# Optimization experiments

Measured on AMD Instinct MI355X. Metric: run time of the kernel, lower is better.

## Reference

```python
import jax, jax.numpy as jnp
import numpy as np

EMB_DIM = 1024
NUM_HEAD = 16
HEAD_DIM = EMB_DIM // NUM_HEAD
B, S = 2, 2048


def setup_inputs() -> dict:
    key = jax.random.key(0)
    ks = jax.random.split(key, 10)
    scale = 1.0 / np.sqrt(EMB_DIM)
    x = jax.random.normal(ks[0], (B, S, EMB_DIM), dtype=jnp.float32)
    # causal mask: 1 = keep, 0 = masked out (torch masked_fill(mask == 0, -inf))
    mask = jnp.tril(jnp.ones((S, S), dtype=jnp.int32))[None, None, :, :]
    def lin(kw, kb):
        W = jax.random.uniform(kw, (EMB_DIM, EMB_DIM), jnp.float32, -scale, scale)
        b = jax.random.uniform(kb, (EMB_DIM,), jnp.float32, -scale, scale)
        return W, b
    Wq, bq = lin(ks[1], ks[2])
    Wk, bk = lin(ks[3], ks[4])
    Wv, bv = lin(ks[5], ks[6])
    Wo, bo = lin(ks[7], ks[8])
    return {"x": x, "mask": mask, "Wq": Wq, "bq": bq, "Wk": Wk, "bk": bk,
            "Wv": Wv, "bv": bv, "Wo": Wo, "bo": bo}


def reference(x, mask, Wq, bq, Wk, bk, Wv, bv, Wo, bo):
    Bsz, Sq, _ = x.shape
    # projections; torch Linear: y = x @ W^T + b
    def proj(W, b):
        y = jnp.einsum('bse,fe->bsf', x, W) + b
        return y.reshape(Bsz, Sq, NUM_HEAD, HEAD_DIM).transpose(0, 2, 1, 3)  # [B,H,S,D]
    q = proj(Wq, bq)
    k = proj(Wk, bk)
    v = proj(Wv, bv)
    scaling = jnp.asarray(HEAD_DIM ** 0.5, x.dtype)
    scores = jnp.einsum('bhqd,bhkd->bhqk', q, k) / scaling  # [B,H,S,S]
    scores = jnp.where(mask == 0, -jnp.inf, scores)
    attn = jax.nn.softmax(scores, axis=-1)
    out = jnp.einsum('bhqk,bhkd->bhqd', attn, v)
    out = out.transpose(0, 2, 1, 3).reshape(Bsz, Sq, EMB_DIM)
    return jnp.einsum('bse,fe->bsf', out, Wo) + bo
```

## Files before the change

kernel.cpp:

```cpp
#include <hip/hip_runtime.h>

typedef unsigned short u16;
typedef __attribute__((ext_vector_type(8))) __bf16 bf16x8;
typedef __attribute__((ext_vector_type(8))) short  short8;
typedef __attribute__((ext_vector_type(4))) short  short4v;
typedef __attribute__((ext_vector_type(4))) float  floatx4;

constexpr int Bc = 2, Sc = 2048, Ec = 1024, Hc = 16, Dc = 64;
constexpr int Mc = Bc * Sc;

#define NEG_BIG (-1.0e30f)
#define QSCALE  0.18033688011112042f

__device__ __forceinline__ u16 f2b(float f) {
  union { float f; unsigned u; } c; c.f = f;
  unsigned u = c.u;
  return (u16)((u + 0x7fffu + ((u >> 16) & 1u)) >> 16);
}
__device__ __forceinline__ u16 f2b_fast(float f) {
  union { float f; unsigned u; } c; c.f = f;
  return (u16)((c.u + 0x8000u) >> 16);
}
__device__ __forceinline__ short8 ld8(const u16* p) { return *(const short8*)p; }

__device__ __forceinline__ floatx4 mfma16(short8 a, short8 b, floatx4 c) {
  return __builtin_amdgcn_mfma_f32_16x16x32_bf16(
      __builtin_bit_cast(bf16x8, a), __builtin_bit_cast(bf16x8, b), c, 0, 0, 0);
}

__device__ __forceinline__ void async16(const u16* g, u16* l) {
  __builtin_amdgcn_global_load_lds(
      (const __attribute__((address_space(1))) void*)g,
      (__attribute__((address_space(3))) void*)l, 16, 0, 0);
}

__global__ __launch_bounds__(256) void cvt_kernel(
    const float* __restrict__ x,  const float* __restrict__ Wq,
    const float* __restrict__ Wk, const float* __restrict__ Wv,
    const float* __restrict__ Wo, u16* __restrict__ dst) {
  const size_t i = ((size_t)blockIdx.x * 256 + threadIdx.x) * 4;
  const int seg = (int)(i >> 20);
  const float* src;
  size_t off;
  if (seg < 4)       { src = x;  off = i; }
  else if (seg == 4) { src = Wq; off = i - ((size_t)4 << 20); }
  else if (seg == 5) { src = Wk; off = i - ((size_t)5 << 20); }
  else if (seg == 6) { src = Wv; off = i - ((size_t)6 << 20); }
  else               { src = Wo; off = i - ((size_t)7 << 20); }
  floatx4 v = *(const floatx4*)(src + off);
  short4v o;
  o[0] = (short)f2b(v[0]); o[1] = (short)f2b(v[1]);
  o[2] = (short)f2b(v[2]); o[3] = (short)f2b(v[3]);
  *(short4v*)(dst + i) = o;
}

__device__ __forceinline__ void gemm128(
    const u16* __restrict__ A, const u16* __restrict__ B, int K,
    int m0, int n0, u16* As, u16* Bs, floatx4 acc[4][4]) {
  const int t = threadIdx.x;
  const int w = t >> 6, lane = t & 63;
  const int wm = w & 1, wn = w >> 1;
  const int quad = lane >> 4, l16 = lane & 15;
  const int r = t >> 2;
  const int c = (t & 3) * 8;

#pragma unroll
  for (int i = 0; i < 4; ++i)
#pragma unroll
    for (int j = 0; j < 4; ++j) acc[i][j] = 0.f;

  for (int k0 = 0; k0 < K; k0 += 32) {
#pragma unroll
    for (int jj = 0; jj < 2; ++jj) {
      async16(A + (size_t)(m0 + jj * 64 + r) * K + k0 + c, As + jj * 2048 + w * 512);
      async16(B + (size_t)(n0 + jj * 64 + r) * K + k0 + c, Bs + jj * 2048 + w * 512);
    }
    __syncthreads();
    short8 af[4], bfr[4];
#pragma unroll
    for (int i = 0; i < 4; ++i)
      af[i]  = *(const short8*)(As + (wm * 64 + i * 16 + l16) * 32 + quad * 8);
#pragma unroll
    for (int j = 0; j < 4; ++j)
      bfr[j] = *(const short8*)(Bs + (wn * 64 + j * 16 + l16) * 32 + quad * 8);
#pragma unroll
    for (int i = 0; i < 4; ++i)
#pragma unroll
      for (int j = 0; j < 4; ++j)
        acc[i][j] = mfma16(af[i], bfr[j], acc[i][j]);
    __syncthreads();
  }
}

__global__ __launch_bounds__(256) void qkv_mm(
    const u16* __restrict__ xb, const u16* __restrict__ Wb,
    const float* __restrict__ bq, const float* __restrict__ bk,
    const float* __restrict__ bv,
    u16* __restrict__ Q, u16* __restrict__ K_, u16* __restrict__ Vt) {
  __shared__ __align__(16) u16 As[4096], Bs[4096];
  const int z = blockIdx.z;
  const u16* W = Wb + ((size_t)z << 20);
  const float* bias = (z == 0) ? bq : (z == 1) ? bk : bv;
  const int m0 = blockIdx.y * 128, n0 = blockIdx.x * 128;

  floatx4 acc[4][4];
  gemm128(xb, W, Ec, m0, n0, As, Bs, acc);

  const int t = threadIdx.x, w = t >> 6, lane = t & 63;
  const int wm = w & 1, wn = w >> 1, quad = lane >> 4, l16 = lane & 15;
#pragma unroll
  for (int i = 0; i < 4; ++i)
#pragma unroll
    for (int j = 0; j < 4; ++j)
#pragma unroll
      for (int rr = 0; rr < 4; ++rr) {
        const int row = m0 + wm * 64 + i * 16 + quad * 4 + rr;
        const int col = n0 + wn * 64 + j * 16 + l16;
        float v = acc[i][j][rr] + bias[col];
        if (z == 0) v *= QSCALE;
        const int bb = row >> 11, s = row & (Sc - 1);
        const int h = col >> 6, d = col & (Dc - 1), bh = bb * Hc + h;
        if (z < 2) ((z == 0) ? Q : K_)[((size_t)bh * Sc + s) * Dc + d] = f2b(v);
        else       Vt[((size_t)bh * Dc + d) * Sc + s] = f2b(v);
      }
}

__global__ __launch_bounds__(256) void proj_mm(
    const u16* __restrict__ O, const u16* __restrict__ Wob,
    const float* __restrict__ bias, float* __restrict__ out) {
  __shared__ __align__(16) u16 As[4096], Bs[4096];
  const int m0 = blockIdx.y * 128, n0 = blockIdx.x * 128;

  floatx4 acc[4][4];
  gemm128(O, Wob, Ec, m0, n0, As, Bs, acc);

  const int t = threadIdx.x, w = t >> 6, lane = t & 63;
  const int wm = w & 1, wn = w >> 1, quad = lane >> 4, l16 = lane & 15;
#pragma unroll
  for (int i = 0; i < 4; ++i)
#pragma unroll
    for (int j = 0; j < 4; ++j)
#pragma unroll
      for (int rr = 0; rr < 4; ++rr) {
        const int row = m0 + wm * 64 + i * 16 + quad * 4 + rr;
        const int col = n0 + wn * 64 + j * 16 + l16;
        out[(size_t)row * Ec + col] = acc[i][j][rr] + bias[col];
      }
}

__global__ __launch_bounds__(256, 4) void attn_kernel(
    const u16* __restrict__ Q, const u16* __restrict__ K,
    const u16* __restrict__ Vt, u16* __restrict__ O) {
  const int qt = 31 - (int)((blockIdx.x + blockIdx.y) & 31);
  const int q0 = qt * 64;
  const int bh = blockIdx.y;
  const int bb = bh >> 4, h = bh & 15;

  const u16* Qh = Q  + (size_t)bh * Sc * Dc;
  const u16* Kh = K  + (size_t)bh * Sc * Dc;
  const u16* Vh = Vt + (size_t)bh * Dc * Sc;

  const int t = threadIdx.x;
  const int w = t >> 6, lane = t & 63;
  const int quad = lane >> 4, l16 = lane & 15;

  __shared__ __align__(16) u16 Ks[8192];
  __shared__ __align__(16) u16 Vs[8192];
  __shared__ __align__(16) u16 Pl[4096];
  u16* const Pw = Pl + w * 1024;

  const int sr = w * 8 + (lane >> 3);
  const int sb = (lane & 7) ^ (lane >> 3);
  const int swz = l16 & 7;

  const u16* qrow_p = Qh + (size_t)(q0 + w * 16 + l16) * Dc;
  const short8 aq0 = ld8(qrow_p + quad * 8);
  const short8 aq1 = ld8(qrow_p + 32 + quad * 8);

  float   lrow[4];
  floatx4 oacc[4];
#pragma unroll
  for (int r = 0; r < 4; ++r) lrow[r] = 0.f;
#pragma unroll
  for (int dt = 0; dt < 4; ++dt) oacc[dt] = 0.f;

  for (int kt = 0; kt <= q0; kt += 128) {
#pragma unroll
    for (int st = 0; st < 2; ++st)
#pragma unroll
      for (int it = 0; it < 2; ++it) {
        const int r = it * 32 + sr;
        async16(Kh + (size_t)(kt + st * 64 + r) * Dc + sb * 8,
                Ks + st * 4096 + it * 2048 + w * 512);
        async16(Vh + (size_t)r * Sc + kt + st * 64 + sb * 8,
                Vs + st * 4096 + it * 2048 + w * 512);
      }
    __syncthreads();

    floatx4 sacc[8];
#pragma unroll
    for (int nt = 0; nt < 8; ++nt) sacc[nt] = 0.f;
#pragma unroll
    for (int ks = 0; ks < 2; ++ks) {
      const short8 a = ks ? aq1 : aq0;
#pragma unroll
      for (int nt = 0; nt < 8; ++nt) {
        const short8 b = *(const short8*)(
            Ks + (nt >> 2) * 4096 + ((nt & 3) * 16 + l16) * 64 +
            (((ks * 4 + quad) ^ swz) * 8));
        sacc[nt] = mfma16(a, b, sacc[nt]);
      }
    }

    const bool diag = (kt + 128 > q0);
    float s2buf[4][4];
#pragma unroll
    for (int r = 0; r < 4; ++r) {
      const int row = quad * 4 + r;
      float sv[8];
#pragma unroll
      for (int nt = 0; nt < 8; ++nt) sv[nt] = sacc[nt][r];
      if (diag) {
        const int qrow = q0 + w * 16 + row;
#pragma unroll
        for (int nt = 0; nt < 8; ++nt)
          if (kt + nt * 16 + l16 > qrow) sv[nt] = NEG_BIG;
      }
      float ls = 0.f;
#pragma unroll
      for (int nt = 0; nt < 8; ++nt) {
        const float pv = exp2f(sv[nt]);
        sv[nt] = pv;
        ls += pv;
      }
      lrow[r] += ls;
      const int sx = row & 7;
#pragma unroll
      for (int j = 0; j < 4; ++j) {
        Pw[row * 64 + (((2 * j + (l16 >> 3)) ^ sx) * 8) + (l16 & 7)] =
            f2b_fast(sv[j]);
        s2buf[r][j] = sv[4 + j];
      }
    }

#pragma unroll
    for (int kc = 0; kc < 2; ++kc) {
      const short8 a = ld8(Pw + l16 * 64 + (((kc * 4 + quad) ^ swz) * 8));
#pragma unroll
      for (int dt = 0; dt < 4; ++dt) {
        const short8 b = *(const short8*)(
            Vs + (dt * 16 + l16) * 64 + (((kc * 4 + quad) ^ swz) * 8));
        oacc[dt] = mfma16(a, b, oacc[dt]);
      }
    }

#pragma unroll
    for (int r = 0; r < 4; ++r) {
      const int row = quad * 4 + r, sx = row & 7;
#pragma unroll
      for (int j = 0; j < 4; ++j)
        Pw[row * 64 + (((2 * j + (l16 >> 3)) ^ sx) * 8) + (l16 & 7)] =
            f2b_fast(s2buf[r][j]);
    }

#pragma unroll
    for (int kc = 0; kc < 2; ++kc) {
      const short8 a = ld8(Pw + l16 * 64 + (((kc * 4 + quad) ^ swz) * 8));
#pragma unroll
      for (int dt = 0; dt < 4; ++dt) {
        const short8 b = *(const short8*)(
            Vs + 4096 + (dt * 16 + l16) * 64 + (((kc * 4 + quad) ^ swz) * 8));
        oacc[dt] = mfma16(a, b, oacc[dt]);
      }
    }
    __syncthreads();
  }

#pragma unroll
  for (int r = 0; r < 4; ++r)
#pragma unroll
    for (int sh = 1; sh < 16; sh <<= 1) lrow[r] += __shfl_xor(lrow[r], sh, 16);

#pragma unroll
  for (int dt = 0; dt < 4; ++dt) {
#pragma unroll
    for (int r = 0; r < 4; ++r) {
      const int qrow = q0 + w * 16 + quad * 4 + r;
      const float ov = oacc[dt][r] / lrow[r];
      O[((size_t)(bb * Sc + qrow)) * Ec + h * Dc + dt * 16 + l16] = f2b(ov);
    }
  }
}

extern "C" void kernel_launch(void* const* d_in, const int* in_sizes, int n_in,
                              void* d_out, int out_size, void* d_ws, size_t ws_size,
                              hipStream_t stream) {
  const float* x  = (const float*)d_in[0];
  const float* Wq = (const float*)d_in[2];
  const float* bq = (const float*)d_in[3];
  const float* Wk = (const float*)d_in[4];
  const float* bk = (const float*)d_in[5];
  const float* Wv = (const float*)d_in[6];
  const float* bv = (const float*)d_in[7];
  const float* Wo = (const float*)d_in[8];
  const float* bo = (const float*)d_in[9];

  const size_t MiE = (size_t)Mc * Ec;
  u16* Q  = (u16*)d_ws;
  u16* K  = Q  + MiE;
  u16* Vt = K  + MiE;
  u16* O  = Vt + MiE;
  u16* xb = O  + MiE;
  u16* Wb = xb + MiE;
  u16* Wob = Wb + ((size_t)3 << 20);

  cvt_kernel<<<8192, 256, 0, stream>>>(x, Wq, Wk, Wv, Wo, xb);
  qkv_mm<<<dim3(Ec / 128, Mc / 128, 3), 256, 0, stream>>>(
      xb, Wb, bq, bk, bv, Q, K, Vt);
  attn_kernel<<<dim3(32, Bc * Hc), 256, 0, stream>>>(Q, K, Vt, O);
  proj_mm<<<dim3(Ec / 128, Mc / 128), 256, 0, stream>>>(O, Wob, bo, (float*)d_out);
}
```

Baseline: 214.8 us.

## Widen GEMM K-tile to 64 with swizzled LDS and snake-order attention blocks

The shared GEMM routine now loads 64-wide K tiles into XOR-swizzled shared memory, halving the number of barrier pairs per GEMM and aiming to avoid LDS bank conflicts on fragment reads. LDS per GEMM block doubles, which may lower occupancy. The attention launch becomes a 1D grid that is remapped in a serpentine order, dispatching the longest causal query tiles first across all heads to balance load. Some variables are renamed to avoid shadowing.

```diff
diff --git a/kernel.cpp b/kernel.cpp
--- a/kernel.cpp
+++ b/kernel.cpp
@@ -61,33 +61,41 @@
   const int w = t >> 6, lane = t & 63;
   const int wm = w & 1, wn = w >> 1;
   const int quad = lane >> 4, l16 = lane & 15;
-  const int r = t >> 2;
-  const int c = (t & 3) * 8;
+  const int swz = l16 & 7;
+  const int lr = lane >> 3;
+  const int sb = (lane & 7) ^ lr;
 
 #pragma unroll
   for (int i = 0; i < 4; ++i)
 #pragma unroll
     for (int j = 0; j < 4; ++j) acc[i][j] = 0.f;
 
-  for (int k0 = 0; k0 < K; k0 += 32) {
-#pragma unroll
-    for (int jj = 0; jj < 2; ++jj) {
-      async16(A + (size_t)(m0 + jj * 64 + r) * K + k0 + c, As + jj * 2048 + w * 512);
-      async16(B + (size_t)(n0 + jj * 64 + r) * K + k0 + c, Bs + jj * 2048 + w * 512);
+  for (int k0 = 0; k0 < K; k0 += 64) {
+#pragma unroll
+    for (int it = 0; it < 4; ++it) {
+      const int chunk = it * 4 + w;
+      const int row = chunk * 8 + lr;
+      async16(A + (size_t)(m0 + row) * K + k0 + sb * 8, As + chunk * 512);
+      async16(B + (size_t)(n0 + row) * K + k0 + sb * 8, Bs + chunk * 512);
     }
     __syncthreads();
-    short8 af[4], bfr[4];
-#pragma unroll
-    for (int i = 0; i < 4; ++i)
-      af[i]  = *(const short8*)(As + (wm * 64 + i * 16 + l16) * 32 + quad * 8);
-#pragma unroll
-    for (int j = 0; j < 4; ++j)
-      bfr[j] = *(const short8*)(Bs + (wn * 64 + j * 16 + l16) * 32 + quad * 8);
-#pragma unroll
-    for (int i = 0; i < 4; ++i)
+#pragma unroll
+    for (int ks = 0; ks < 2; ++ks) {
+      short8 af[4], bfr[4];
+#pragma unroll
+      for (int i = 0; i < 4; ++i)
+        af[i] = *(const short8*)(
+            As + (wm * 64 + i * 16 + l16) * 64 + (((ks * 4 + quad) ^ swz) * 8));
 #pragma unroll
       for (int j = 0; j < 4; ++j)
-        acc[i][j] = mfma16(af[i], bfr[j], acc[i][j]);
+        bfr[j] = *(const short8*)(
+            Bs + (wn * 64 + j * 16 + l16) * 64 + (((ks * 4 + quad) ^ swz) * 8));
+#pragma unroll
+      for (int i = 0; i < 4; ++i)
+#pragma unroll
+        for (int j = 0; j < 4; ++j)
+          acc[i][j] = mfma16(af[i], bfr[j], acc[i][j]);
+    }
     __syncthreads();
   }
 }
@@ -97,7 +105,7 @@
     const float* __restrict__ bq, const float* __restrict__ bk,
     const float* __restrict__ bv,
     u16* __restrict__ Q, u16* __restrict__ K_, u16* __restrict__ Vt) {
-  __shared__ __align__(16) u16 As[4096], Bs[4096];
+  __shared__ __align__(16) u16 As[8192], Bs[8192];
   const int z = blockIdx.z;
   const u16* W = Wb + ((size_t)z << 20);
   const float* bias = (z == 0) ? bq : (z == 1) ? bk : bv;
@@ -128,7 +136,7 @@
 __global__ __launch_bounds__(256) void proj_mm(
     const u16* __restrict__ O, const u16* __restrict__ Wob,
     const float* __restrict__ bias, float* __restrict__ out) {
-  __shared__ __align__(16) u16 As[4096], Bs[4096];
+  __shared__ __align__(16) u16 As[8192], Bs[8192];
   const int m0 = blockIdx.y * 128, n0 = blockIdx.x * 128;
 
   floatx4 acc[4][4];
@@ -151,9 +159,12 @@
 __global__ __launch_bounds__(256, 4) void attn_kernel(
     const u16* __restrict__ Q, const u16* __restrict__ K,
     const u16* __restrict__ Vt, u16* __restrict__ O) {
-  const int qt = 31 - (int)((blockIdx.x + blockIdx.y) & 31);
+  const int b = blockIdx.x;
+  const int s_ = b >> 8, c_ = b & 255;
+  const int rank = (s_ << 8) + ((s_ & 1) ? (255 - c_) : c_);
+  const int qt = 31 - (rank >> 5);
   const int q0 = qt * 64;
-  const int bh = blockIdx.y;
+  const int bh = rank & 31;
   const int bb = bh >> 4, h = bh & 15;
 
   const u16* Qh = Q  + (size_t)bh * Sc * Dc;
@@ -205,10 +216,10 @@
       const short8 a = ks ? aq1 : aq0;
 #pragma unroll
       for (int nt = 0; nt < 8; ++nt) {
-        const short8 b = *(const short8*)(
+        const short8 b2 = *(const short8*)(
             Ks + (nt >> 2) * 4096 + ((nt & 3) * 16 + l16) * 64 +
             (((ks * 4 + quad) ^ swz) * 8));
-        sacc[nt] = mfma16(a, b, sacc[nt]);
+        sacc[nt] = mfma16(a, b2, sacc[nt]);
       }
     }
 
@@ -248,9 +259,9 @@
       const short8 a = ld8(Pw + l16 * 64 + (((kc * 4 + quad) ^ swz) * 8));
 #pragma unroll
       for (int dt = 0; dt < 4; ++dt) {
-        const short8 b = *(const short8*)(
+        const short8 b2 = *(const short8*)(
             Vs + (dt * 16 + l16) * 64 + (((kc * 4 + quad) ^ swz) * 8));
-        oacc[dt] = mfma16(a, b, oacc[dt]);
+        oacc[dt] = mfma16(a, b2, oacc[dt]);
       }
     }
 
@@ -268,9 +279,9 @@
       const short8 a = ld8(Pw + l16 * 64 + (((kc * 4 + quad) ^ swz) * 8));
 #pragma unroll
       for (int dt = 0; dt < 4; ++dt) {
-        const short8 b = *(const short8*)(
+        const short8 b2 = *(const short8*)(
             Vs + 4096 + (dt * 16 + l16) * 64 + (((kc * 4 + quad) ^ swz) * 8));
-        oacc[dt] = mfma16(a, b, oacc[dt]);
+        oacc[dt] = mfma16(a, b2, oacc[dt]);
       }
     }
     __syncthreads();
@@ -317,6 +328,6 @@
   cvt_kernel<<<8192, 256, 0, stream>>>(x, Wq, Wk, Wv, Wo, xb);
   qkv_mm<<<dim3(Ec / 128, Mc / 128, 3), 256, 0, stream>>>(
       xb, Wb, bq, bk, bv, Q, K, Vt);
-  attn_kernel<<<dim3(32, Bc * Hc), 256, 0, stream>>>(Q, K, Vt, O);
+  attn_kernel<<<dim3(1024), 256, 0, stream>>>(Q, K, Vt, O);
   proj_mm<<<dim3(Ec / 128, Mc / 128), 256, 0, stream>>>(O, Wob, bo, (float*)d_out);
 }
```

After: 220.2 us. +2.5%, slower.

## Split attention key tiles across two warp groups and snake-order block scheduling

Applied to the files above, without the earlier changes.

The attention kernel now runs 512 threads per block: four waves per 64-key half of each 128-key tile, so each wave handles half the keys instead of serialising both halves. Partial output accumulators and row sums from the second wave group are merged through shared memory at the end. The grid is flattened to 1D with a serpentine ordering that interleaves heavy and light causal query tiles to balance load across CUs. This adds extra LDS use, an extra barrier and a reduction step, and raises occupancy demands through the launch bounds.

```diff
diff --git a/kernel.cpp b/kernel.cpp
--- a/kernel.cpp
+++ b/kernel.cpp
@@ -148,12 +148,15 @@
       }
 }
 
-__global__ __launch_bounds__(256, 4) void attn_kernel(
+__global__ __launch_bounds__(512, 6) void attn_kernel(
     const u16* __restrict__ Q, const u16* __restrict__ K,
     const u16* __restrict__ Vt, u16* __restrict__ O) {
-  const int qt = 31 - (int)((blockIdx.x + blockIdx.y) & 31);
+  const int b = blockIdx.x;
+  const int s_ = b >> 8, c_ = b & 255;
+  const int rank = (s_ << 8) + ((s_ & 1) ? (255 - c_) : c_);
+  const int qt = 31 - (rank >> 5);
   const int q0 = qt * 64;
-  const int bh = blockIdx.y;
+  const int bh = rank & 31;
   const int bb = bh >> 4, h = bh & 15;
 
   const u16* Qh = Q  + (size_t)bh * Sc * Dc;
@@ -162,18 +165,19 @@
 
   const int t = threadIdx.x;
   const int w = t >> 6, lane = t & 63;
+  const int wq = w & 3, wk = w >> 2;
   const int quad = lane >> 4, l16 = lane & 15;
 
   __shared__ __align__(16) u16 Ks[8192];
   __shared__ __align__(16) u16 Vs[8192];
-  __shared__ __align__(16) u16 Pl[4096];
+  __shared__ __align__(16) u16 Pl[8192];
   u16* const Pw = Pl + w * 1024;
 
-  const int sr = w * 8 + (lane >> 3);
-  const int sb = (lane & 7) ^ (lane >> 3);
+  const int lr = lane >> 3;
+  const int sb = (lane & 7) ^ lr;
   const int swz = l16 & 7;
 
-  const u16* qrow_p = Qh + (size_t)(q0 + w * 16 + l16) * Dc;
+  const u16* qrow_p = Qh + (size_t)(q0 + wq * 16 + l16) * Dc;
   const short8 aq0 = ld8(qrow_p + quad * 8);
   const short8 aq1 = ld8(qrow_p + 32 + quad * 8);
 
@@ -186,49 +190,45 @@
 
   for (int kt = 0; kt <= q0; kt += 128) {
 #pragma unroll
-    for (int st = 0; st < 2; ++st)
-#pragma unroll
-      for (int it = 0; it < 2; ++it) {
-        const int r = it * 32 + sr;
-        async16(Kh + (size_t)(kt + st * 64 + r) * Dc + sb * 8,
-                Ks + st * 4096 + it * 2048 + w * 512);
-        async16(Vh + (size_t)r * Sc + kt + st * 64 + sb * 8,
-                Vs + st * 4096 + it * 2048 + w * 512);
-      }
+    for (int cc = 0; cc < 2; ++cc) {
+      const int ch = w * 2 + cc;
+      const int g  = (ch >> 3) * 64 + (ch & 7) * 8 + lr;
+      async16(Kh + (size_t)(kt + g) * Dc + sb * 8, Ks + ch * 512);
+      async16(Vh + (size_t)((ch & 7) * 8 + lr) * Sc + kt + (ch >> 3) * 64 + sb * 8,
+              Vs + ch * 512);
+    }
     __syncthreads();
 
-    floatx4 sacc[8];
-#pragma unroll
-    for (int nt = 0; nt < 8; ++nt) sacc[nt] = 0.f;
+    floatx4 sacc[4];
+#pragma unroll
+    for (int nt = 0; nt < 4; ++nt) sacc[nt] = 0.f;
 #pragma unroll
     for (int ks = 0; ks < 2; ++ks) {
       const short8 a = ks ? aq1 : aq0;
 #pragma unroll
-      for (int nt = 0; nt < 8; ++nt) {
-        const short8 b = *(const short8*)(
-            Ks + (nt >> 2) * 4096 + ((nt & 3) * 16 + l16) * 64 +
-            (((ks * 4 + quad) ^ swz) * 8));
-        sacc[nt] = mfma16(a, b, sacc[nt]);
-      }
-    }
-
-    const bool diag = (kt + 128 > q0);
-    float s2buf[4][4];
+      for (int nt = 0; nt < 4; ++nt) {
+        const short8 b2 = *(const short8*)(
+            Ks + wk * 4096 + (nt * 16 + l16) * 64 + (((ks * 4 + quad) ^ swz) * 8));
+        sacc[nt] = mfma16(a, b2, sacc[nt]);
+      }
+    }
+
+    const bool diag = (kt + wk * 64 + 64 > q0);
 #pragma unroll
     for (int r = 0; r < 4; ++r) {
       const int row = quad * 4 + r;
-      float sv[8];
-#pragma unroll
-      for (int nt = 0; nt < 8; ++nt) sv[nt] = sacc[nt][r];
+      float sv[4];
+#pragma unroll
+      for (int nt = 0; nt < 4; ++nt) sv[nt] = sacc[nt][r];
       if (diag) {
-        const int qrow = q0 + w * 16 + row;
-#pragma unroll
-        for (int nt = 0; nt < 8; ++nt)
-          if (kt + nt * 16 + l16 > qrow) sv[nt] = NEG_BIG;
+        const int qrow = q0 + wq * 16 + row;
+#pragma unroll
+        for (int nt = 0; nt < 4; ++nt)
+          if (kt + wk * 64 + nt * 16 + l16 > qrow) sv[nt] = NEG_BIG;
       }
       float ls = 0.f;
 #pragma unroll
-      for (int nt = 0; nt < 8; ++nt) {
+      for (int nt = 0; nt < 4; ++nt) {
         const float pv = exp2f(sv[nt]);
         sv[nt] = pv;
         ls += pv;
@@ -236,11 +236,9 @@
       lrow[r] += ls;
       const int sx = row & 7;
 #pragma unroll
-      for (int j = 0; j < 4; ++j) {
-        Pw[row * 64 + (((2 * j + (l16 >> 3)) ^ sx) * 8) + (l16 & 7)] =
-            f2b_fast(sv[j]);
-        s2buf[r][j] = sv[4 + j];
-      }
+      for (int nt = 0; nt < 4; ++nt)
+        Pw[row * 64 + (((2 * nt + (l16 >> 3)) ^ sx) * 8) + (l16 & 7)] =
+            f2b_fast(sv[nt]);
     }
 
 #pragma unroll
@@ -248,47 +246,46 @@
       const short8 a = ld8(Pw + l16 * 64 + (((kc * 4 + quad) ^ swz) * 8));
 #pragma unroll
       for (int dt = 0; dt < 4; ++dt) {
-        const short8 b = *(const short8*)(
-            Vs + (dt * 16 + l16) * 64 + (((kc * 4 + quad) ^ swz) * 8));
-        oacc[dt] = mfma16(a, b, oacc[dt]);
-      }
-    }
-
-#pragma unroll
-    for (int r = 0; r < 4; ++r) {
-      const int row = quad * 4 + r, sx = row & 7;
-#pragma unroll
-      for (int j = 0; j < 4; ++j)
-        Pw[row * 64 + (((2 * j + (l16 >> 3)) ^ sx) * 8) + (l16 & 7)] =
-            f2b_fast(s2buf[r][j]);
-    }
-
-#pragma unroll
-    for (int kc = 0; kc < 2; ++kc) {
-      const short8 a = ld8(Pw + l16 * 64 + (((kc * 4 + quad) ^ swz) * 8));
-#pragma unroll
-      for (int dt = 0; dt < 4; ++dt) {
-        const short8 b = *(const short8*)(
-            Vs + 4096 + (dt * 16 + l16) * 64 + (((kc * 4 + quad) ^ swz) * 8));
-        oacc[dt] = mfma16(a, b, oacc[dt]);
+        const short8 b2 = *(const short8*)(
+            Vs + wk * 4096 + (dt * 16 + l16) * 64 + (((kc * 4 + quad) ^ swz) * 8));
+        oacc[dt] = mfma16(a, b2, oacc[dt]);
       }
     }
     __syncthreads();
   }
 
-#pragma unroll
-  for (int r = 0; r < 4; ++r)
-#pragma unroll
-    for (int sh = 1; sh < 16; sh <<= 1) lrow[r] += __shfl_xor(lrow[r], sh, 16);
-
-#pragma unroll
-  for (int dt = 0; dt < 4; ++dt) {
+  float* const Om = (float*)Ks;
+  float* const Lm = (float*)Vs;
+  if (wk == 1) {
+#pragma unroll
+    for (int dt = 0; dt < 4; ++dt)
+#pragma unroll
+      for (int r = 0; r < 4; ++r)
+        Om[wq * 1024 + dt * 256 + r * 64 + lane] = oacc[dt][r];
+#pragma unroll
+    for (int r = 0; r < 4; ++r) Lm[wq * 256 + r * 64 + lane] = lrow[r];
+  }
+  __syncthreads();
+  if (wk == 0) {
+#pragma unroll
+    for (int dt = 0; dt < 4; ++dt)
+#pragma unroll
+      for (int r = 0; r < 4; ++r)
+        oacc[dt][r] += Om[wq * 1024 + dt * 256 + r * 64 + lane];
 #pragma unroll
     for (int r = 0; r < 4; ++r) {
-      const int qrow = q0 + w * 16 + quad * 4 + r;
-      const float ov = oacc[dt][r] / lrow[r];
-      O[((size_t)(bb * Sc + qrow)) * Ec + h * Dc + dt * 16 + l16] = f2b(ov);
-    }
+      lrow[r] += Lm[wq * 256 + r * 64 + lane];
+#pragma unroll
+      for (int sh = 1; sh < 16; sh <<= 1) lrow[r] += __shfl_xor(lrow[r], sh, 16);
+    }
+#pragma unroll
+    for (int dt = 0; dt < 4; ++dt)
+#pragma unroll
+      for (int r = 0; r < 4; ++r) {
+        const int qrow = q0 + wq * 16 + quad * 4 + r;
+        const float ov = oacc[dt][r] / lrow[r];
+        O[((size_t)(bb * Sc + qrow)) * Ec + h * Dc + dt * 16 + l16] = f2b(ov);
+      }
   }
 }
 
@@ -317,6 +314,6 @@
   cvt_kernel<<<8192, 256, 0, stream>>>(x, Wq, Wk, Wv, Wo, xb);
   qkv_mm<<<dim3(Ec / 128, Mc / 128, 3), 256, 0, stream>>>(
       xb, Wb, bq, bk, bv, Q, K, Vt);
-  attn_kernel<<<dim3(32, Bc * Hc), 256, 0, stream>>>(Q, K, Vt, O);
+  attn_kernel<<<dim3(1024), 512, 0, stream>>>(Q, K, Vt, O);
   proj_mm<<<dim3(Ec / 128, Mc / 128), 256, 0, stream>>>(O, Wob, bo, (float*)d_out);
 }
```

Result: slower. 262.2 us (+22.1%).
